# Kernel tuning notes

Measured on AMD Instinct MI355X. Metric: run time of the kernel, lower is better.

The kernel has to match this reference:

```python
import jax, jax.numpy as jnp
import numpy as np

N_NODES = 100000
N_EDGES = 1600000
D_FEAT = 64
K = 8
AVG_DEGREE = 16


def setup_inputs() -> dict:
    key = jax.random.key(0)
    k1, k2, k3, k4 = jax.random.split(key, 4)
    x = jax.random.normal(k1, (N_NODES, D_FEAT), dtype=jnp.float32)
    # scale weights ~1/degree so repeated propagation stays bounded
    edge_weight = jax.random.uniform(k2, (N_EDGES,), dtype=jnp.float32) / AVG_DEGREE
    src = jax.random.randint(k3, (N_EDGES,), 0, N_NODES)
    dst = jax.random.randint(k4, (N_EDGES,), 0, N_NODES)
    return {"x": x, "edge_weight": edge_weight, "src": src, "dst": dst}


def reference(x, edge_weight, src, dst):
    # Prop.forward: x = spmm(adj, x) repeated K times; returned value is adj^K @ x.
    # (The in-place y.add_(x) accumulator mutates the input tensor but is not returned.)
    n = x.shape[0]
    w = edge_weight[:, None]  # [E,1]

    def step(h, _):
        # one spmm: out[dst] += w * h[src]
        h = jax.ops.segment_sum(w * h[src], dst, num_segments=n)
        return h, None

    x, _ = jax.lax.scan(step, x, None, length=K)
    return x
```

## Files before the change

kernel.cpp:

```cpp
#include <hip/hip_runtime.h>

#define N_NODES 100000
#define N_EDGES 1600000
#define D_FEAT  64
#define K_STEPS 8
#define NB_SCAN ((N_NODES + 255) / 256)

typedef unsigned long long u64;
typedef float f4 __attribute__((ext_vector_type(4)));

__global__ void k_zero(int* __restrict__ p, int n) {
    int i = blockIdx.x * blockDim.x + threadIdx.x;
    if (i < n) p[i] = 0;
}

__global__ void k_hist(const int* __restrict__ dst, int* __restrict__ counts,
                       int* __restrict__ rank, int n) {
    int i = blockIdx.x * blockDim.x + threadIdx.x;
    if (i < n) rank[i] = atomicAdd(&counts[dst[i]], 1);
}

__global__ void k_bsum(const int* __restrict__ counts, int* __restrict__ blockSums, int n) {
    __shared__ int ws[4];
    int t = threadIdx.x;
    int i = blockIdx.x * 256 + t;
    int c = (i < n) ? counts[i] : 0;
    for (int off = 32; off; off >>= 1) c += __shfl_down(c, off);
    if ((t & 63) == 0) ws[t >> 6] = c;
    __syncthreads();
    if (t == 0) blockSums[blockIdx.x] = ws[0] + ws[1] + ws[2] + ws[3];
}

__global__ void k_sscan(const int* __restrict__ blockSums, int* __restrict__ blockPrefix,
                        int* __restrict__ offsets, int nb, int n) {
    __shared__ int sh[512];
    int t = threadIdx.x;
    int v = (t < nb) ? blockSums[t] : 0;
    sh[t] = v;
    __syncthreads();
    for (int off = 1; off < 512; off <<= 1) {
        int u = (t >= off) ? sh[t - off] : 0;
        __syncthreads();
        sh[t] += u;
        __syncthreads();
    }
    if (t < nb) blockPrefix[t] = sh[t] - v;
    if (t == 511) offsets[n] = sh[511];
}

__global__ void k_bscan(const int* __restrict__ counts, const int* __restrict__ blockPrefix,
                        int* __restrict__ offsets, int n) {
    __shared__ int sh[256];
    int t = threadIdx.x;
    int i = blockIdx.x * 256 + t;
    int c = (i < n) ? counts[i] : 0;
    sh[t] = c;
    __syncthreads();
    for (int off = 1; off < 256; off <<= 1) {
        int u = (t >= off) ? sh[t - off] : 0;
        __syncthreads();
        sh[t] += u;
        __syncthreads();
    }
    int excl = sh[t] - c + blockPrefix[blockIdx.x];
    if (i < n) offsets[i] = excl;
}

__global__ void k_scatter(const int* __restrict__ src, const int* __restrict__ dst,
                          const float* __restrict__ w, const int* __restrict__ offsets,
                          const int* __restrict__ rank, u64* __restrict__ csr, int n) {
    int i = blockIdx.x * blockDim.x + threadIdx.x;
    if (i < n) {
        int d = dst[i];
        int pos = offsets[d] + rank[i];
        csr[pos] = ((u64)__float_as_uint(w[i]) << 32) | (unsigned)src[i];
    }
}

__global__ __launch_bounds__(256)
void k_prop(const float* __restrict__ hin, float* __restrict__ hout,
            const int* __restrict__ offsets, const u64* __restrict__ csr, int n) {
    int wave = (blockIdx.x * blockDim.x + threadIdx.x) >> 6;
    int lane = threadIdx.x & 63;
    if (wave >= n) return;
    int b = offsets[wave];
    int e = offsets[wave + 1];
    int eg = lane >> 3;
    int fl = lane & 7;
    f4 a0 = {0.f, 0.f, 0.f, 0.f};
    f4 a1 = {0.f, 0.f, 0.f, 0.f};
    f4 c0 = {0.f, 0.f, 0.f, 0.f};
    f4 c1 = {0.f, 0.f, 0.f, 0.f};
    for (int i = b + eg; i < e; i += 16) {
        int  iB  = i + 8;
        bool okB = iB < e;
        u64 pA = csr[i];
        u64 pB = okB ? csr[iB] : 0;
        int   sA = (int)(pA & 0xffffffffu);
        float wA = __uint_as_float((unsigned)(pA >> 32));
        int   sB = okB ? (int)(pB & 0xffffffffu) : 0;
        float wB = okB ? __uint_as_float((unsigned)(pB >> 32)) : 0.f;
        const f4* rA = reinterpret_cast<const f4*>(&hin[((size_t)sA << 6) + (fl << 3)]);
        const f4* rB = reinterpret_cast<const f4*>(&hin[((size_t)sB << 6) + (fl << 3)]);
        f4 vA0 = rA[0], vA1 = rA[1];
        f4 vB0 = rB[0], vB1 = rB[1];
        a0.x = fmaf(wA, vA0.x, a0.x); a0.y = fmaf(wA, vA0.y, a0.y);
        a0.z = fmaf(wA, vA0.z, a0.z); a0.w = fmaf(wA, vA0.w, a0.w);
        a1.x = fmaf(wA, vA1.x, a1.x); a1.y = fmaf(wA, vA1.y, a1.y);
        a1.z = fmaf(wA, vA1.z, a1.z); a1.w = fmaf(wA, vA1.w, a1.w);
        c0.x = fmaf(wB, vB0.x, c0.x); c0.y = fmaf(wB, vB0.y, c0.y);
        c0.z = fmaf(wB, vB0.z, c0.z); c0.w = fmaf(wB, vB0.w, c0.w);
        c1.x = fmaf(wB, vB1.x, c1.x); c1.y = fmaf(wB, vB1.y, c1.y);
        c1.z = fmaf(wB, vB1.z, c1.z); c1.w = fmaf(wB, vB1.w, c1.w);
    }
    a0.x += c0.x; a0.y += c0.y; a0.z += c0.z; a0.w += c0.w;
    a1.x += c1.x; a1.y += c1.y; a1.z += c1.z; a1.w += c1.w;
    #pragma unroll
    for (int off = 8; off < 64; off <<= 1) {
        a0.x += __shfl_xor(a0.x, off);
        a0.y += __shfl_xor(a0.y, off);
        a0.z += __shfl_xor(a0.z, off);
        a0.w += __shfl_xor(a0.w, off);
        a1.x += __shfl_xor(a1.x, off);
        a1.y += __shfl_xor(a1.y, off);
        a1.z += __shfl_xor(a1.z, off);
        a1.w += __shfl_xor(a1.w, off);
    }
    if (eg == 0) {
        f4* o = reinterpret_cast<f4*>(&hout[((size_t)wave << 6) + (fl << 3)]);
        o[0] = a0;
        o[1] = a1;
    }
}

extern "C" void kernel_launch(void* const* d_in, const int* in_sizes, int n_in,
                              void* d_out, int out_size, void* d_ws, size_t ws_size,
                              hipStream_t stream) {
    const float* x   = (const float*)d_in[0];
    const float* ew  = (const float*)d_in[1];
    const int*   src = (const int*)d_in[2];
    const int*   dst = (const int*)d_in[3];
    float* out = (float*)d_out;

    float* hA         = (float*)d_ws;
    int*   rank       = (int*)d_ws;
    u64*   csr        = (u64*)(hA + (size_t)N_NODES * D_FEAT);
    int*   offsets    = (int*)(csr + N_EDGES);
    int*   counts     = offsets + (N_NODES + 1);
    int*   blockSums  = counts + N_NODES;
    int*   blockPref  = blockSums + NB_SCAN;

    k_zero<<<(N_NODES + 255) / 256, 256, 0, stream>>>(counts, N_NODES);
    k_hist<<<(N_EDGES + 255) / 256, 256, 0, stream>>>(dst, counts, rank, N_EDGES);
    k_bsum<<<NB_SCAN, 256, 0, stream>>>(counts, blockSums, N_NODES);
    k_sscan<<<1, 512, 0, stream>>>(blockSums, blockPref, offsets, NB_SCAN, N_NODES);
    k_bscan<<<NB_SCAN, 256, 0, stream>>>(counts, blockPref, offsets, N_NODES);
    k_scatter<<<(N_EDGES + 255) / 256, 256, 0, stream>>>(src, dst, ew, offsets, rank,
                                                         csr, N_EDGES);

    const int prop_grid = (N_NODES * 64 + 255) / 256;
    const float* in = x;
    for (int k = 0; k < K_STEPS; ++k) {
        float* o = (k & 1) ? out : hA;
        k_prop<<<prop_grid, 256, 0, stream>>>(in, o, offsets, csr, N_NODES);
        in = o;
    }
}
```

Before: 553.2 us.

## Build CSR via two-level bucketed partition with LDS histograms instead of global atomics

Replaces the global-atomic per-node histogram and rank-based scatter with a two-pass bucket partition. Edges are first counted into 128-node buckets per 4096-edge chunk using shared-memory atomics, then scanned and partitioned into a staging buffer. Each bucket is then sorted into the final CSR by a per-bucket block that uses LDS counting. The aim is to remove contended global atomics and random scattered writes from CSR construction, at the cost of an extra pass over the staging buffer and more kernel launches. It also swaps the order of two independent FMAs in the propagation kernel, which has no speed effect.

```diff
diff --git a/kernel.cpp b/kernel.cpp
--- a/kernel.cpp
+++ b/kernel.cpp
@@ -4,56 +4,73 @@
 #define N_EDGES 1600000
 #define D_FEAT  64
 #define K_STEPS 8
-#define NB_SCAN ((N_NODES + 255) / 256)
+
+#define CHUNK   4096
+#define EPT     16
+#define BSHIFT  7
+#define NBUCK   ((N_NODES + 127) >> 7)
+#define NBLK_P  ((N_EDGES + CHUNK - 1) / CHUNK)
+#define NSCAN   (NBUCK * NBLK_P)
+#define NB_BS   ((NSCAN + 255) / 256)
 
 typedef unsigned long long u64;
 typedef float f4 __attribute__((ext_vector_type(4)));
 
-__global__ void k_zero(int* __restrict__ p, int n) {
-    int i = blockIdx.x * blockDim.x + threadIdx.x;
-    if (i < n) p[i] = 0;
-}
-
-__global__ void k_hist(const int* __restrict__ dst, int* __restrict__ counts,
-                       int* __restrict__ rank, int n) {
-    int i = blockIdx.x * blockDim.x + threadIdx.x;
-    if (i < n) rank[i] = atomicAdd(&counts[dst[i]], 1);
-}
-
-__global__ void k_bsum(const int* __restrict__ counts, int* __restrict__ blockSums, int n) {
+__global__ __launch_bounds__(256)
+void k_p1_count(const int* __restrict__ dst, int* __restrict__ gcount, int n) {
+    __shared__ int lh[NBUCK];
+    for (int j = threadIdx.x; j < NBUCK; j += 256) lh[j] = 0;
+    __syncthreads();
+    int base = blockIdx.x * CHUNK + threadIdx.x;
+    #pragma unroll
+    for (int k = 0; k < EPT; ++k) {
+        int i = base + k * 256;
+        if (i < n) atomicAdd(&lh[dst[i] >> BSHIFT], 1);
+    }
+    __syncthreads();
+    for (int j = threadIdx.x; j < NBUCK; j += 256)
+        gcount[j * NBLK_P + blockIdx.x] = lh[j];
+}
+
+__global__ void k_bsum(const int* __restrict__ a, int* __restrict__ blockSums, int n) {
     __shared__ int ws[4];
     int t = threadIdx.x;
     int i = blockIdx.x * 256 + t;
-    int c = (i < n) ? counts[i] : 0;
+    int c = (i < n) ? a[i] : 0;
     for (int off = 32; off; off >>= 1) c += __shfl_down(c, off);
     if ((t & 63) == 0) ws[t >> 6] = c;
     __syncthreads();
     if (t == 0) blockSums[blockIdx.x] = ws[0] + ws[1] + ws[2] + ws[3];
 }
 
-__global__ void k_sscan(const int* __restrict__ blockSums, int* __restrict__ blockPrefix,
-                        int* __restrict__ offsets, int nb, int n) {
-    __shared__ int sh[512];
-    int t = threadIdx.x;
-    int v = (t < nb) ? blockSums[t] : 0;
-    sh[t] = v;
-    __syncthreads();
-    for (int off = 1; off < 512; off <<= 1) {
+__global__ void k_sscan2(const int* __restrict__ blockSums, int* __restrict__ blockPrefix,
+                         int nb) {
+    __shared__ int sh[1024];
+    int t = threadIdx.x;
+    const int CH = (nb + 1023) / 1024;
+    int b0 = t * CH;
+    int s = 0;
+    for (int k = 0; k < CH; ++k) { int i = b0 + k; if (i < nb) s += blockSums[i]; }
+    sh[t] = s;
+    __syncthreads();
+    for (int off = 1; off < 1024; off <<= 1) {
         int u = (t >= off) ? sh[t - off] : 0;
         __syncthreads();
         sh[t] += u;
         __syncthreads();
     }
-    if (t < nb) blockPrefix[t] = sh[t] - v;
-    if (t == 511) offsets[n] = sh[511];
-}
-
-__global__ void k_bscan(const int* __restrict__ counts, const int* __restrict__ blockPrefix,
-                        int* __restrict__ offsets, int n) {
+    int run = (t == 0) ? 0 : sh[t - 1];
+    for (int k = 0; k < CH; ++k) {
+        int i = b0 + k;
+        if (i < nb) { int c = blockSums[i]; blockPrefix[i] = run; run += c; }
+    }
+}
+
+__global__ void k_bscan(int* __restrict__ a, const int* __restrict__ blockPrefix, int n) {
     __shared__ int sh[256];
     int t = threadIdx.x;
     int i = blockIdx.x * 256 + t;
-    int c = (i < n) ? counts[i] : 0;
+    int c = (i < n) ? a[i] : 0;
     sh[t] = c;
     __syncthreads();
     for (int off = 1; off < 256; off <<= 1) {
@@ -63,18 +80,68 @@
         __syncthreads();
     }
     int excl = sh[t] - c + blockPrefix[blockIdx.x];
-    if (i < n) offsets[i] = excl;
-}
-
-__global__ void k_scatter(const int* __restrict__ src, const int* __restrict__ dst,
-                          const float* __restrict__ w, const int* __restrict__ offsets,
-                          const int* __restrict__ rank, u64* __restrict__ csr, int n) {
-    int i = blockIdx.x * blockDim.x + threadIdx.x;
-    if (i < n) {
-        int d = dst[i];
-        int pos = offsets[d] + rank[i];
-        csr[pos] = ((u64)__float_as_uint(w[i]) << 32) | (unsigned)src[i];
-    }
+    if (i < n) a[i] = excl;
+}
+
+__global__ __launch_bounds__(256)
+void k_p3_part(const int* __restrict__ src, const int* __restrict__ dst,
+               const float* __restrict__ w, const int* __restrict__ gcount,
+               u64* __restrict__ partSW, int* __restrict__ partDst, int n) {
+    __shared__ int lc[NBUCK];
+    for (int j = threadIdx.x; j < NBUCK; j += 256)
+        lc[j] = gcount[j * NBLK_P + blockIdx.x];
+    __syncthreads();
+    int base = blockIdx.x * CHUNK + threadIdx.x;
+    #pragma unroll
+    for (int k = 0; k < EPT; ++k) {
+        int i = base + k * 256;
+        if (i < n) {
+            int d = dst[i];
+            int pos = atomicAdd(&lc[d >> BSHIFT], 1);
+            partSW[pos]  = ((u64)__float_as_uint(w[i]) << 32) | (unsigned)src[i];
+            partDst[pos] = d;
+        }
+    }
+}
+
+__global__ __launch_bounds__(256)
+void k_p4_csr(const u64* __restrict__ partSW, const int* __restrict__ partDst,
+              const int* __restrict__ gcount, int* __restrict__ offsets,
+              u64* __restrict__ csr, int n) {
+    __shared__ int lcnt[128];
+    __shared__ int sh[128];
+    int b = blockIdx.x;
+    int t = threadIdx.x;
+    int dstBase = b << BSHIFT;
+    int bstart = gcount[b * NBLK_P];
+    int bend   = (b == NBUCK - 1) ? N_EDGES : gcount[(b + 1) * NBLK_P];
+    if (t < 128) lcnt[t] = 0;
+    __syncthreads();
+    for (int i = bstart + t; i < bend; i += 256)
+        atomicAdd(&lcnt[partDst[i] - dstBase], 1);
+    __syncthreads();
+    int c = (t < 128) ? lcnt[t] : 0;
+    if (t < 128) sh[t] = c;
+    __syncthreads();
+    for (int off = 1; off < 128; off <<= 1) {
+        int u = (t >= off && t < 128) ? sh[t - off] : 0;
+        __syncthreads();
+        if (t < 128) sh[t] += u;
+        __syncthreads();
+    }
+    if (t < 128) {
+        int excl = sh[t] - c;
+        int v = dstBase + t;
+        if (v < n) offsets[v] = bstart + excl;
+        lcnt[t] = excl;
+    }
+    __syncthreads();
+    for (int i = bstart + t; i < bend; i += 256) {
+        int ld = partDst[i] - dstBase;
+        int r = atomicAdd(&lcnt[ld], 1);
+        csr[bstart + r] = partSW[i];
+    }
+    if (b == 0 && t == 0) offsets[n] = N_EDGES;
 }
 
 __global__ __launch_bounds__(256)
@@ -111,7 +178,7 @@
         c0.x = fmaf(wB, vB0.x, c0.x); c0.y = fmaf(wB, vB0.y, c0.y);
         c0.z = fmaf(wB, vB0.z, c0.z); c0.w = fmaf(wB, vB0.w, c0.w);
         c1.x = fmaf(wB, vB1.x, c1.x); c1.y = fmaf(wB, vB1.y, c1.y);
-        c1.z = fmaf(wB, vB1.z, c1.z); c1.w = fmaf(wB, vB1.w, c1.w);
+        c1.w = fmaf(wB, vB1.w, c1.w); c1.z = fmaf(wB, vB1.z, c1.z);
     }
     a0.x += c0.x; a0.y += c0.y; a0.z += c0.z; a0.w += c0.w;
     a1.x += c1.x; a1.y += c1.y; a1.z += c1.z; a1.w += c1.w;
@@ -142,21 +209,21 @@
     const int*   dst = (const int*)d_in[3];
     float* out = (float*)d_out;
 
-    float* hA         = (float*)d_ws;
-    int*   rank       = (int*)d_ws;
-    u64*   csr        = (u64*)(hA + (size_t)N_NODES * D_FEAT);
-    int*   offsets    = (int*)(csr + N_EDGES);
-    int*   counts     = offsets + (N_NODES + 1);
-    int*   blockSums  = counts + N_NODES;
-    int*   blockPref  = blockSums + NB_SCAN;
-
-    k_zero<<<(N_NODES + 255) / 256, 256, 0, stream>>>(counts, N_NODES);
-    k_hist<<<(N_EDGES + 255) / 256, 256, 0, stream>>>(dst, counts, rank, N_EDGES);
-    k_bsum<<<NB_SCAN, 256, 0, stream>>>(counts, blockSums, N_NODES);
-    k_sscan<<<1, 512, 0, stream>>>(blockSums, blockPref, offsets, NB_SCAN, N_NODES);
-    k_bscan<<<NB_SCAN, 256, 0, stream>>>(counts, blockPref, offsets, N_NODES);
-    k_scatter<<<(N_EDGES + 255) / 256, 256, 0, stream>>>(src, dst, ew, offsets, rank,
-                                                         csr, N_EDGES);
+    float* hA        = (float*)d_ws;
+    u64*   partSW    = (u64*)d_ws;
+    int*   partDst   = (int*)(partSW + N_EDGES);
+    int*   gcount    = partDst + N_EDGES;
+    u64*   csr       = (u64*)(hA + (size_t)N_NODES * D_FEAT);
+    int*   offsets   = (int*)(csr + N_EDGES);
+    int*   blockSums = offsets + (N_NODES + 1);
+    int*   blockPref = blockSums + NB_BS;
+
+    k_p1_count<<<NBLK_P, 256, 0, stream>>>(dst, gcount, N_EDGES);
+    k_bsum    <<<NB_BS, 256, 0, stream>>>(gcount, blockSums, NSCAN);
+    k_sscan2  <<<1, 1024, 0, stream>>>(blockSums, blockPref, NB_BS);
+    k_bscan   <<<NB_BS, 256, 0, stream>>>(gcount, blockPref, NSCAN);
+    k_p3_part <<<NBLK_P, 256, 0, stream>>>(src, dst, ew, gcount, partSW, partDst, N_EDGES);
+    k_p4_csr  <<<NBUCK, 256, 0, stream>>>(partSW, partDst, gcount, offsets, csr, N_NODES);
 
     const int prop_grid = (N_NODES * 64 + 255) / 256;
     const float* in = x;
```

Result: faster. 514.4 us (-7.0%).
